# Kernel optimization log

Measured on AMD Instinct MI355X. Metric: run time of the kernel, lower is better.

The kernel has to match this reference:

```python
import jax, jax.numpy as jnp
import numpy as np

NEG_SLOPE = 0.2  # PyG GATConv default negative_slope


def gat_conv(h_in, src, dst, W, a_src, a_dst, bias, concat):
    """PyG GATConv: linear -> per-edge attention -> segment softmax -> scatter-add.
    h_in: [N, Fin]; W: [heads*C, Fin]; a_src/a_dst: [heads, C]; bias: [heads*C] or [C].
    add_self_loops=True (PyG default)."""
    N = h_in.shape[0]
    heads, C = a_src.shape
    loop = jnp.arange(N, dtype=src.dtype)
    s = jnp.concatenate([src, loop])
    d = jnp.concatenate([dst, loop])
    h = (h_in @ W.T).reshape(N, heads, C)          # [N, H, C]
    al_s = (h * a_src).sum(-1)                      # [N, H]
    al_d = (h * a_dst).sum(-1)                      # [N, H]
    e = jax.nn.leaky_relu(al_s[s] + al_d[d], NEG_SLOPE)  # [E, H]
    emax = jax.ops.segment_max(e, d, num_segments=N)     # every node has a self loop
    ex = jnp.exp(e - emax[d])
    denom = jax.ops.segment_sum(ex, d, num_segments=N)
    alpha = ex / denom[d]                           # [E, H]
    msg = alpha[:, :, None] * h[s]                  # [E, H, C]
    out = jax.ops.segment_sum(msg, d, num_segments=N)    # [N, H, C]
    if concat:
        out = out.reshape(N, heads * C)
    else:
        out = out.mean(axis=1)
    return out + bias


def setup_inputs() -> dict:
    key = jax.random.key(0)
    ks = jax.random.split(key, 14)
    B, N, T = 1, 20000, 4
    E = 320000
    HID, HEADS, OUT = 64, 4, 64
    sc = 0.1
    x = jax.random.normal(ks[0], (B, N, T), dtype=jnp.float32)
    edge_index = jax.random.randint(ks[1], (2, E), 0, N, dtype=jnp.int64)
    time_idx = jnp.arange(T, dtype=jnp.float32).reshape(T, 1)
    return {
        "x": x,
        "edge_index": edge_index,
        "time_idx": time_idx,
        "Wt": jax.random.normal(ks[2], (HID, 1), jnp.float32) * sc,
        "bt": jnp.zeros((HID,), jnp.float32),
        "Wf": jax.random.normal(ks[3], (HID, 1), jnp.float32) * sc,
        "bf": jnp.zeros((HID,), jnp.float32),
        "W1": jax.random.normal(ks[4], (HEADS * HID, HID), jnp.float32) * sc,
        "a_src1": jax.random.normal(ks[5], (HEADS, HID), jnp.float32) * sc,
        "a_dst1": jax.random.normal(ks[6], (HEADS, HID), jnp.float32) * sc,
        "b1": jnp.zeros((HEADS * HID,), jnp.float32),
        "temporal_attention": jnp.ones((T,), jnp.float32),
        "W2": jax.random.normal(ks[7], (OUT, HEADS * HID), jnp.float32) * sc,
        "a_src2": jax.random.normal(ks[8], (1, OUT), jnp.float32) * sc,
        "a_dst2": jax.random.normal(ks[9], (1, OUT), jnp.float32) * sc,
        "b2": jnp.zeros((OUT,), jnp.float32),
    }


def reference(x, edge_index, time_idx, Wt, bt, Wf, bf, W1, a_src1, a_dst1, b1,
              temporal_attention, W2, a_src2, a_dst2, b2):
    B, N, T = x.shape  # features dim == time_steps
    src, dst = edge_index[0], edge_index[1]
    time_emb = time_idx @ Wt.T + bt                 # [T, hidden]
    tw = jax.nn.softmax(temporal_attention)         # [T]
    combined = jnp.zeros((B * N, a_src1.shape[0] * a_src1.shape[1]), x.dtype)
    for t in range(T):  # small static time loop, as in original
        feats = x[:, :, t].reshape(-1, 1)           # [B*N, 1]
        emb = feats @ Wf.T + bf + time_emb[t]       # [B*N, hidden]
        h = gat_conv(emb, src, dst, W1, a_src1, a_dst1, b1, concat=True)
        combined = combined + tw[t] * jax.nn.relu(h)  # dropout is identity in eval
    out = gat_conv(combined, src, dst, W2, a_src2, a_dst2, b2, concat=False)
    return out.reshape(B, N, -1)
```

## Files before the change

kernel.cpp:

```cpp
#include <hip/hip_runtime.h>
#include <hip/hip_bf16.h>

#define NEG 0.2f
#define NELL 64

#define P_U   0
#define P_W   256
#define P_PS  1280
#define P_PD  1284
#define P_QS  1288
#define P_QD  1304
#define P_TW  1320
#define P_WT  1324
#define P_CNT 2560

typedef __bf16 bf16x8 __attribute__((ext_vector_type(8)));
typedef float  f32x4  __attribute__((ext_vector_type(4)));

__device__ __forceinline__ float lrelu(float v){ return v > 0.f ? v : NEG*v; }
__device__ __forceinline__ unsigned short f2bf(float f){
    unsigned u = __float_as_uint(f);
    unsigned r = u + 0x7fffu + ((u >> 16) & 1u);
    return (unsigned short)(r >> 16);
}

__global__ void preK(const float* time_idx, const float* Wt, const float* bt,
                     const float* Wf, const float* bf, const float* W1,
                     const float* as1, const float* ad1, const float* b1,
                     const float* ta, const float* W2,
                     float* P, unsigned short* W2bf, int* deg, int N)
{
    int tid = threadIdx.x;
    if (blockIdx.x != 0){
        int i0 = (blockIdx.x - 1)*256 + tid;
        int stride = (gridDim.x - 1)*256;
        for (int i = i0; i < N; i += stride) deg[i] = 0;
        for (int i = i0; i < 16384; i += stride) W2bf[i] = f2bf(W2[i]);
        return;
    }
    __shared__ float W1p[256][65];
    for (int i = tid; i < 16384; i += 256){
        int r = i >> 6, c = i & 63;
        W1p[r][c] = W1[i];
    }
    __syncthreads();
    const float* wrow = W1p[tid];
    float uu = 0.f;
    for (int k = 0; k < 64; ++k) uu += wrow[k]*Wf[k];
    P[P_U + tid] = uu;
    for (int t = 0; t < 4; ++t){
        float ti = time_idx[t];
        float vv = 0.f;
        for (int k = 0; k < 64; ++k) vv += wrow[k]*(bf[k] + ti*Wt[k] + bt[k]);
        P[P_W + t*256 + tid] = vv + b1[tid];
    }
    __syncthreads();
    if (tid < 4){
        int h = tid; float ps=0.f, pd=0.f;
        for (int c = 0; c < 64; ++c){
            float uv = P[P_U + h*64 + c];
            ps += uv * as1[h*64+c];
            pd += uv * ad1[h*64+c];
        }
        P[P_PS+h]=ps; P[P_PD+h]=pd;
    }
    if (tid < 16){
        int t = tid >> 2, h = tid & 3;
        float qs=0.f, qd=0.f;
        for (int c = 0; c < 64; ++c){
            float v = P[P_W + t*256 + h*64 + c] - b1[h*64+c];
            qs += v * as1[h*64+c];
            qd += v * ad1[h*64+c];
        }
        P[P_QS + t*4 + h] = qs;
        P[P_QD + t*4 + h] = qd;
    }
    if (tid == 0){
        float m = ta[0];
        for (int t = 1; t < 4; ++t) m = fmaxf(m, ta[t]);
        float s = 0.f, e[4];
        for (int t = 0; t < 4; ++t){ e[t] = __expf(ta[t]-m); s += e[t]; }
        for (int t = 0; t < 4; ++t) P[P_TW+t] = e[t]/s;
    }
    __syncthreads();
    for (int idx = tid; idx < 1024; idx += 256){
        int c = idx >> 2, t = idx & 3;
        P[P_WT + idx] = P[P_W + t*256 + c];
    }
}

__global__ void ellK(const int* ei, int E, int* deg, int* ell){
    int e = blockIdx.x*256 + threadIdx.x;
    if (e >= E) return;
    int d = ei[E+e];
    int pos = atomicAdd(&deg[d], 1);
    if (pos < NELL) ell[d*NELL + pos] = ei[e];
}

__launch_bounds__(256)
__global__ void gat1h2K(const float* x, const int* deg, const int* ell,
                        const float* P, const unsigned short* W2bfg,
                        const float* as2, const float* ad2,
                        unsigned short* h2bf, float* als2, float* ald2, int N)
{
    __shared__ unsigned short Abf[64*264];
    __shared__ float4 Sl[64][4];
    __shared__ float  Ul[256];
    __shared__ float4 WTl[256];
    __shared__ float  Pl[44];
    int tid = threadIdx.x;
    Ul[tid] = P[P_U + tid];
    WTl[tid] = reinterpret_cast<const float4*>(P + P_WT)[tid];
    if (tid < 44) Pl[tid] = P[P_PS + tid];
    __syncthreads();

    int nl = tid >> 2, t = tid & 3;
    int n  = blockIdx.x*64 + nl;
    {
        float s_out[4] = {0.f,0.f,0.f,0.f};
        if (n < N){
            float xn = x[n*4 + t];
            float ps[4], qsum[4], den[4], num[4];
            #pragma unroll
            for (int h = 0; h < 4; ++h){
                ps[h]   = Pl[h];
                qsum[h] = Pl[8 + t*4 + h] + xn*Pl[4 + h] + Pl[24 + t*4 + h];
                float ex = __expf(lrelu(xn*ps[h] + qsum[h]));
                den[h] = ex; num[h] = ex*xn;
            }
            int dgn = min(deg[n], NELL);
            const int* row = ell + n*NELL;
            int j = 0;
            for (; j + 4 <= dgn; j += 4){
                float v0 = x[row[j]*4 + t];
                float v1 = x[row[j+1]*4 + t];
                float v2 = x[row[j+2]*4 + t];
                float v3 = x[row[j+3]*4 + t];
                #pragma unroll
                for (int h = 0; h < 4; ++h){
                    float e0 = __expf(lrelu(v0*ps[h] + qsum[h]));
                    float e1 = __expf(lrelu(v1*ps[h] + qsum[h]));
                    float e2 = __expf(lrelu(v2*ps[h] + qsum[h]));
                    float e3 = __expf(lrelu(v3*ps[h] + qsum[h]));
                    den[h] += (e0 + e1) + (e2 + e3);
                    num[h] += e0*v0 + e1*v1 + e2*v2 + e3*v3;
                }
            }
            for (; j < dgn; ++j){
                float v = x[row[j]*4 + t];
                #pragma unroll
                for (int h = 0; h < 4; ++h){
                    float ex = __expf(lrelu(v*ps[h] + qsum[h]));
                    den[h] += ex; num[h] += ex*v;
                }
            }
            #pragma unroll
            for (int h = 0; h < 4; ++h) s_out[h] = num[h]/den[h];
        }
        #pragma unroll
        for (int h = 0; h < 4; ++h)
            reinterpret_cast<float*>(&Sl[nl][h])[t] = s_out[h];
    }
    __syncthreads();

    {
        float tw0 = Pl[40], tw1 = Pl[41], tw2 = Pl[42], tw3 = Pl[43];
        int q = t;
        float4 s4 = Sl[nl][q];
        unsigned int* arow = reinterpret_cast<unsigned int*>(&Abf[nl*264 + q*64]);
        #pragma unroll 8
        for (int jj = 0; jj < 64; jj += 2){
            int c = q*64 + jj;
            float4 wa = WTl[c], wb = WTl[c+1];
            float ua = Ul[c], ub = Ul[c+1];
            float v0 = tw0*fmaxf(s4.x*ua + wa.x, 0.f) + tw1*fmaxf(s4.y*ua + wa.y, 0.f)
                     + tw2*fmaxf(s4.z*ua + wa.z, 0.f) + tw3*fmaxf(s4.w*ua + wa.w, 0.f);
            float v1 = tw0*fmaxf(s4.x*ub + wb.x, 0.f) + tw1*fmaxf(s4.y*ub + wb.y, 0.f)
                     + tw2*fmaxf(s4.z*ub + wb.z, 0.f) + tw3*fmaxf(s4.w*ub + wb.w, 0.f);
            arow[jj>>1] = (unsigned)f2bf(v0) | ((unsigned)f2bf(v1) << 16);
        }
    }
    __syncthreads();

    int w = tid >> 6, lane = tid & 63, lr = lane & 15, lhi = lane >> 4;
    int r0 = w*16;
    bf16x8 a[8];
    #pragma unroll
    for (int kk = 0; kk < 8; ++kk)
        a[kk] = *reinterpret_cast<const bf16x8*>(&Abf[(r0+lr)*264 + kk*32 + lhi*8]);
    float s1[4] = {0.f,0.f,0.f,0.f}, s2[4] = {0.f,0.f,0.f,0.f};
    int gbase = blockIdx.x*64 + r0 + lhi*4;
    #pragma unroll
    for (int nt = 0; nt < 4; ++nt){
        f32x4 acc = {0.f,0.f,0.f,0.f};
        const unsigned short* bp = W2bfg + (nt*16 + lr)*256 + lhi*8;
        #pragma unroll
        for (int kk = 0; kk < 8; ++kk){
            bf16x8 b = *reinterpret_cast<const bf16x8*>(bp + kk*32);
            acc = __builtin_amdgcn_mfma_f32_16x16x32_bf16(a[kk], b, acc, 0, 0, 0);
        }
        float oas = as2[nt*16 + lr], oad = ad2[nt*16 + lr];
        #pragma unroll
        for (int r = 0; r < 4; ++r){
            int g = gbase + r;
            if (g < N) h2bf[(size_t)g*64 + nt*16 + lr] = f2bf(acc[r]);
            s1[r] += acc[r]*oas;
            s2[r] += acc[r]*oad;
        }
    }
    #pragma unroll
    for (int r = 0; r < 4; ++r){
        float v1 = s1[r], v2 = s2[r];
        #pragma unroll
        for (int off = 8; off > 0; off >>= 1){
            v1 += __shfl_xor(v1, off);
            v2 += __shfl_xor(v2, off);
        }
        int g = gbase + r;
        if (lr == 0 && g < N){ als2[g] = v1; ald2[g] = v2; }
    }
}

__launch_bounds__(256)
__global__ void attnpvK(const unsigned short* h2bf, const float* als2, const float* ald2,
                        const int* deg, const int* ell, const float* b2,
                        float* out, int N)
{
    __shared__ int   sbuf[8][32];
    __shared__ float wbuf[8][32];
    int hw = threadIdx.x >> 5, lane = threadIdx.x & 31;
    int n = blockIdx.x*8 + hw;
    if (n >= N) return;
    float aldn = ald2[n];
    int dgn = min(deg[n], NELL);
    const int* row = ell + n*NELL;
    float sw = __expf(lrelu(als2[n] + aldn));
    float den = sw;
    unsigned us = reinterpret_cast<const unsigned*>(h2bf + ((size_t)n<<6))[lane];
    float acc0 = sw * __uint_as_float(us << 16);
    float acc1 = sw * __uint_as_float(us & 0xffff0000u);
    for (int base = 0; base < dgn; base += 32){
        int cnt = min(32, dgn - base);
        int j = base + lane;
        int s = 0; float ex = 0.f;
        if (j < dgn){ s = row[j]; ex = __expf(lrelu(als2[s] + aldn)); }
        sbuf[hw][lane] = s; wbuf[hw][lane] = ex;
        float sx = ex;
        #pragma unroll
        for (int off = 16; off; off >>= 1) sx += __shfl_xor(sx, off);
        den += sx;
        int i = 0;
        for (; i + 4 <= cnt; i += 4){
            int   s0 = sbuf[hw][i],   s1 = sbuf[hw][i+1], s2 = sbuf[hw][i+2], s3 = sbuf[hw][i+3];
            float w0 = wbuf[hw][i],   w1 = wbuf[hw][i+1], w2 = wbuf[hw][i+2], w3 = wbuf[hw][i+3];
            unsigned g0 = reinterpret_cast<const unsigned*>(h2bf + ((size_t)s0<<6))[lane];
            unsigned g1 = reinterpret_cast<const unsigned*>(h2bf + ((size_t)s1<<6))[lane];
            unsigned g2 = reinterpret_cast<const unsigned*>(h2bf + ((size_t)s2<<6))[lane];
            unsigned g3 = reinterpret_cast<const unsigned*>(h2bf + ((size_t)s3<<6))[lane];
            acc0 += w0*__uint_as_float(g0 << 16);
            acc1 += w0*__uint_as_float(g0 & 0xffff0000u);
            acc0 += w1*__uint_as_float(g1 << 16);
            acc1 += w1*__uint_as_float(g1 & 0xffff0000u);
            acc0 += w2*__uint_as_float(g2 << 16);
            acc1 += w2*__uint_as_float(g2 & 0xffff0000u);
            acc0 += w3*__uint_as_float(g3 << 16);
            acc1 += w3*__uint_as_float(g3 & 0xffff0000u);
        }
        for (; i < cnt; ++i){
            float wv = wbuf[hw][i];
            unsigned g = reinterpret_cast<const unsigned*>(h2bf + ((size_t)sbuf[hw][i]<<6))[lane];
            acc0 += wv*__uint_as_float(g << 16);
            acc1 += wv*__uint_as_float(g & 0xffff0000u);
        }
    }
    float rd = 1.f/den;
    int c = lane*2;
    float2 o;
    o.x = acc0*rd + b2[c];
    o.y = acc1*rd + b2[c+1];
    reinterpret_cast<float2*>(out + (size_t)n*64)[lane] = o;
}

extern "C" void kernel_launch(void* const* d_in, const int* in_sizes, int n_in,
                              void* d_out, int out_size, void* d_ws, size_t ws_size,
                              hipStream_t stream)
{
    const float* x        = (const float*)d_in[0];
    const int*   ei       = (const int*)  d_in[1];
    const float* time_idx = (const float*)d_in[2];
    const float* Wt       = (const float*)d_in[3];
    const float* bt       = (const float*)d_in[4];
    const float* Wf       = (const float*)d_in[5];
    const float* bf       = (const float*)d_in[6];
    const float* W1       = (const float*)d_in[7];
    const float* as1      = (const float*)d_in[8];
    const float* ad1      = (const float*)d_in[9];
    const float* b1       = (const float*)d_in[10];
    const float* ta       = (const float*)d_in[11];
    const float* W2       = (const float*)d_in[12];
    const float* as2      = (const float*)d_in[13];
    const float* ad2      = (const float*)d_in[14];
    const float* b2       = (const float*)d_in[15];

    int N = in_sizes[0] / 4;
    int E = in_sizes[1] / 2;

    char* w = (char*)d_ws;
    auto al = [](size_t v){ return (v + 255) & ~(size_t)255; };
    size_t off = 0;
    float* P     = (float*)(w + off); off = al(off + P_CNT*sizeof(float));
    unsigned short* W2bf = (unsigned short*)(w + off); off = al(off + 16384*sizeof(unsigned short));
    int*   deg   = (int*)  (w + off); off = al(off + (size_t)N*sizeof(int));
    int*   ell   = (int*)  (w + off); off = al(off + (size_t)N*NELL*sizeof(int));
    unsigned short* h2bf = (unsigned short*)(w + off); off = al(off + (size_t)N*64*sizeof(unsigned short));
    float* als2  = (float*)(w + off); off = al(off + (size_t)N*sizeof(float));
    float* ald2  = (float*)(w + off); off = al(off + (size_t)N*sizeof(float));
    (void)off; (void)ws_size; (void)n_in; (void)out_size;

    preK<<<40, 256, 0, stream>>>(time_idx, Wt, bt, Wf, bf, W1, as1, ad1, b1, ta, W2, P, W2bf, deg, N);
    ellK<<<(E + 255)/256, 256, 0, stream>>>(ei, E, deg, ell);
    gat1h2K<<<(N + 63)/64, 256, 0, stream>>>(x, deg, ell, P, W2bf, as2, ad2, h2bf, als2, ald2, N);
    attnpvK<<<(N + 7)/8, 256, 0, stream>>>(h2bf, als2, ald2, deg, ell, b2, (float*)d_out, N);
}
```

Measured before the change: 73.40 us.

## Fuse ELL build, layer-1 GAT and layer-2 attention into one persistent kernel

Merges three kernels (ELL construction, the fused layer-1/h2 projection, and layer-2 attention aggregation) into a single kernel of 32-node tiles. Two hierarchical global barriers built from atomics, leaf counters plus a root, replace the kernel boundaries. Each block caches its tile's ELL rows and degrees in LDS and reuses its own als/ald values, which removes launch gaps and some global reloads. The grid barrier is only safe if all 625 blocks are co-resident, which launch_bounds(256,3) is meant to help with. If they are not, the spin guard can break out early and produce incorrect results, and the barriers themselves add spin overhead.

```diff
diff --git a/kernel.cpp b/kernel.cpp
--- a/kernel.cpp
+++ b/kernel.cpp
@@ -3,6 +3,10 @@
 
 #define NEG 0.2f
 #define NELL 64
+#define TILE 32
+#define NT 256
+#define NLEAF 64
+#define LSTRIDE 16
 
 #define P_U   0
 #define P_W   256
@@ -23,23 +27,45 @@
     unsigned r = u + 0x7fffu + ((u >> 16) & 1u);
     return (unsigned short)(r >> 16);
 }
+__device__ __forceinline__ float bflo(unsigned u){ return __uint_as_float(u << 16); }
+__device__ __forceinline__ float bfhi(unsigned u){ return __uint_as_float(u & 0xffff0000u); }
+
+__device__ __forceinline__ void gbar(int* leaf, int* root, int nblk, int phase){
+    __syncthreads();
+    if (threadIdx.x == 0){
+        __builtin_amdgcn_fence(__ATOMIC_RELEASE, "agent");
+        int li = blockIdx.x & (NLEAF-1);
+        int share = (nblk - li + NLEAF - 1) >> 6;
+        int lv = __hip_atomic_fetch_add(&leaf[li*LSTRIDE], 1, __ATOMIC_RELAXED, __HIP_MEMORY_SCOPE_AGENT) + 1;
+        if (lv == phase*share)
+            __hip_atomic_fetch_add(root, 1, __ATOMIC_RELAXED, __HIP_MEMORY_SCOPE_AGENT);
+        int guard = 0;
+        while (__hip_atomic_load(root, __ATOMIC_RELAXED, __HIP_MEMORY_SCOPE_AGENT) < phase*NLEAF){
+            __builtin_amdgcn_s_sleep(4);
+            if (++guard > 100000000) break;
+        }
+        __builtin_amdgcn_fence(__ATOMIC_ACQUIRE, "agent");
+    }
+    __syncthreads();
+}
 
 __global__ void preK(const float* time_idx, const float* Wt, const float* bt,
                      const float* Wf, const float* bf, const float* W1,
                      const float* as1, const float* ad1, const float* b1,
                      const float* ta, const float* W2,
-                     float* P, unsigned short* W2bf, int* deg, int N)
+                     float* P, unsigned short* W2bf, int* deg, int* barL, int N)
 {
     int tid = threadIdx.x;
     if (blockIdx.x != 0){
-        int i0 = (blockIdx.x - 1)*256 + tid;
-        int stride = (gridDim.x - 1)*256;
+        int i0 = (blockIdx.x - 1)*NT + tid;
+        int stride = (gridDim.x - 1)*NT;
         for (int i = i0; i < N; i += stride) deg[i] = 0;
+        for (int i = i0; i < NLEAF*LSTRIDE + 16; i += stride) barL[i] = 0;
         for (int i = i0; i < 16384; i += stride) W2bf[i] = f2bf(W2[i]);
         return;
     }
     __shared__ float W1p[256][65];
-    for (int i = tid; i < 16384; i += 256){
+    for (int i = tid; i < 16384; i += NT){
         int r = i >> 6, c = i & 63;
         W1p[r][c] = W1[i];
     }
@@ -83,202 +109,214 @@
         for (int t = 0; t < 4; ++t) P[P_TW+t] = e[t]/s;
     }
     __syncthreads();
-    for (int idx = tid; idx < 1024; idx += 256){
+    for (int idx = tid; idx < 1024; idx += NT){
         int c = idx >> 2, t = idx & 3;
         P[P_WT + idx] = P[P_W + t*256 + c];
     }
 }
 
-__global__ void ellK(const int* ei, int E, int* deg, int* ell){
-    int e = blockIdx.x*256 + threadIdx.x;
-    if (e >= E) return;
-    int d = ei[E+e];
-    int pos = atomicAdd(&deg[d], 1);
-    if (pos < NELL) ell[d*NELL + pos] = ei[e];
-}
-
-__launch_bounds__(256)
-__global__ void gat1h2K(const float* x, const int* deg, const int* ell,
-                        const float* P, const unsigned short* W2bfg,
-                        const float* as2, const float* ad2,
-                        unsigned short* h2bf, float* als2, float* ald2, int N)
+__global__ __launch_bounds__(NT, 3)
+void megaK(const float* x, const int* ei, int E, int N,
+           const float* P, const unsigned short* W2bfg,
+           const float* as2, const float* ad2, const float* b2,
+           int* deg, int* ell, unsigned short* h2bf, float* als2, float* ald2,
+           int* leaf, int* root, float* out, int nblk)
 {
-    __shared__ unsigned short Abf[64*264];
-    __shared__ float4 Sl[64][4];
+    __shared__ unsigned short Abf[TILE*264];
+    __shared__ float  Slf[TILE][4][4];
+    __shared__ float4 WTl[256];
     __shared__ float  Ul[256];
-    __shared__ float4 WTl[256];
     __shared__ float  Pl[44];
-    int tid = threadIdx.x;
+    __shared__ int    ellL[TILE][NELL];
+    __shared__ int    degL[TILE];
+    __shared__ float  redL[2][2][TILE];
+    __shared__ int    sbufB[8][32];
+    __shared__ float  wbufB[8][32];
+
+    int tid = threadIdx.x, bid = blockIdx.x;
+    int n0 = bid*TILE;
+
     Ul[tid] = P[P_U + tid];
     WTl[tid] = reinterpret_cast<const float4*>(P + P_WT)[tid];
     if (tid < 44) Pl[tid] = P[P_PS + tid];
-    __syncthreads();
-
-    int nl = tid >> 2, t = tid & 3;
-    int n  = blockIdx.x*64 + nl;
+
+    for (int e = bid*NT + tid; e < E; e += nblk*NT){
+        int d = ei[E+e];
+        int pos = atomicAdd(&deg[d], 1);
+        if (pos < NELL) ell[d*NELL + pos] = ei[e];
+    }
+    gbar(leaf, root, nblk, 1);
+
+    for (int i = tid; i < TILE*NELL; i += NT){
+        int r = i >> 6;
+        if (n0 + r < N) ellL[r][i & 63] = ell[(n0+r)*NELL + (i & 63)];
+    }
+    if (tid < TILE){
+        degL[tid] = (n0 + tid < N) ? min(deg[n0+tid], NELL) : 0;
+    }
+    __syncthreads();
+
     {
-        float s_out[4] = {0.f,0.f,0.f,0.f};
+        int nl = tid >> 3, t = (tid >> 1) & 3, hp = tid & 1;
+        int n = n0 + nl;
+        int h0 = hp*2, h1 = h0 + 1;
+        float o0 = 0.f, o1 = 0.f;
         if (n < N){
             float xn = x[n*4 + t];
-            float ps[4], qsum[4], den[4], num[4];
-            #pragma unroll
-            for (int h = 0; h < 4; ++h){
-                ps[h]   = Pl[h];
-                qsum[h] = Pl[8 + t*4 + h] + xn*Pl[4 + h] + Pl[24 + t*4 + h];
-                float ex = __expf(lrelu(xn*ps[h] + qsum[h]));
-                den[h] = ex; num[h] = ex*xn;
-            }
-            int dgn = min(deg[n], NELL);
-            const int* row = ell + n*NELL;
+            float ps0 = Pl[h0], ps1 = Pl[h1];
+            float q0 = Pl[8 + t*4 + h0] + xn*Pl[4 + h0] + Pl[24 + t*4 + h0];
+            float q1 = Pl[8 + t*4 + h1] + xn*Pl[4 + h1] + Pl[24 + t*4 + h1];
+            float e0 = __expf(lrelu(xn*ps0 + q0));
+            float e1 = __expf(lrelu(xn*ps1 + q1));
+            float den0 = e0, num0 = e0*xn, den1 = e1, num1 = e1*xn;
+            int dgn = degL[nl];
             int j = 0;
             for (; j + 4 <= dgn; j += 4){
-                float v0 = x[row[j]*4 + t];
-                float v1 = x[row[j+1]*4 + t];
-                float v2 = x[row[j+2]*4 + t];
-                float v3 = x[row[j+3]*4 + t];
-                #pragma unroll
-                for (int h = 0; h < 4; ++h){
-                    float e0 = __expf(lrelu(v0*ps[h] + qsum[h]));
-                    float e1 = __expf(lrelu(v1*ps[h] + qsum[h]));
-                    float e2 = __expf(lrelu(v2*ps[h] + qsum[h]));
-                    float e3 = __expf(lrelu(v3*ps[h] + qsum[h]));
-                    den[h] += (e0 + e1) + (e2 + e3);
-                    num[h] += e0*v0 + e1*v1 + e2*v2 + e3*v3;
-                }
+                int s0 = ellL[nl][j], s1 = ellL[nl][j+1], s2 = ellL[nl][j+2], s3 = ellL[nl][j+3];
+                float v0 = x[s0*4 + t], v1 = x[s1*4 + t], v2 = x[s2*4 + t], v3 = x[s3*4 + t];
+                float a0 = __expf(lrelu(v0*ps0 + q0)), c0 = __expf(lrelu(v0*ps1 + q1));
+                float a1 = __expf(lrelu(v1*ps0 + q0)), c1 = __expf(lrelu(v1*ps1 + q1));
+                float a2 = __expf(lrelu(v2*ps0 + q0)), c2 = __expf(lrelu(v2*ps1 + q1));
+                float a3 = __expf(lrelu(v3*ps0 + q0)), c3 = __expf(lrelu(v3*ps1 + q1));
+                den0 += (a0 + a1) + (a2 + a3);
+                num0 += a0*v0 + a1*v1 + a2*v2 + a3*v3;
+                den1 += (c0 + c1) + (c2 + c3);
+                num1 += c0*v0 + c1*v1 + c2*v2 + c3*v3;
             }
             for (; j < dgn; ++j){
-                float v = x[row[j]*4 + t];
-                #pragma unroll
-                for (int h = 0; h < 4; ++h){
-                    float ex = __expf(lrelu(v*ps[h] + qsum[h]));
-                    den[h] += ex; num[h] += ex*v;
-                }
-            }
-            #pragma unroll
-            for (int h = 0; h < 4; ++h) s_out[h] = num[h]/den[h];
-        }
-        #pragma unroll
-        for (int h = 0; h < 4; ++h)
-            reinterpret_cast<float*>(&Sl[nl][h])[t] = s_out[h];
+                float v = x[ellL[nl][j]*4 + t];
+                float a = __expf(lrelu(v*ps0 + q0)), c = __expf(lrelu(v*ps1 + q1));
+                den0 += a; num0 += a*v;
+                den1 += c; num1 += c*v;
+            }
+            o0 = num0/den0; o1 = num1/den1;
+        }
+        Slf[nl][h0][t] = o0;
+        Slf[nl][h1][t] = o1;
     }
     __syncthreads();
 
     {
+        int nl = tid >> 3, q = tid & 7;
         float tw0 = Pl[40], tw1 = Pl[41], tw2 = Pl[42], tw3 = Pl[43];
-        int q = t;
-        float4 s4 = Sl[nl][q];
-        unsigned int* arow = reinterpret_cast<unsigned int*>(&Abf[nl*264 + q*64]);
+        unsigned* arow = reinterpret_cast<unsigned*>(&Abf[nl*264 + q*32]);
         #pragma unroll 8
-        for (int jj = 0; jj < 64; jj += 2){
-            int c = q*64 + jj;
+        for (int jj = 0; jj < 32; jj += 2){
+            int c = q*32 + jj;
+            int h = c >> 6;
+            float sx = Slf[nl][h][0], sy = Slf[nl][h][1], sz = Slf[nl][h][2], sw = Slf[nl][h][3];
             float4 wa = WTl[c], wb = WTl[c+1];
             float ua = Ul[c], ub = Ul[c+1];
-            float v0 = tw0*fmaxf(s4.x*ua + wa.x, 0.f) + tw1*fmaxf(s4.y*ua + wa.y, 0.f)
-                     + tw2*fmaxf(s4.z*ua + wa.z, 0.f) + tw3*fmaxf(s4.w*ua + wa.w, 0.f);
-            float v1 = tw0*fmaxf(s4.x*ub + wb.x, 0.f) + tw1*fmaxf(s4.y*ub + wb.y, 0.f)
-                     + tw2*fmaxf(s4.z*ub + wb.z, 0.f) + tw3*fmaxf(s4.w*ub + wb.w, 0.f);
+            float v0 = tw0*fmaxf(sx*ua + wa.x, 0.f) + tw1*fmaxf(sy*ua + wa.y, 0.f)
+                     + tw2*fmaxf(sz*ua + wa.z, 0.f) + tw3*fmaxf(sw*ua + wa.w, 0.f);
+            float v1 = tw0*fmaxf(sx*ub + wb.x, 0.f) + tw1*fmaxf(sy*ub + wb.y, 0.f)
+                     + tw2*fmaxf(sz*ub + wb.z, 0.f) + tw3*fmaxf(sw*ub + wb.w, 0.f);
             arow[jj>>1] = (unsigned)f2bf(v0) | ((unsigned)f2bf(v1) << 16);
         }
     }
     __syncthreads();
 
-    int w = tid >> 6, lane = tid & 63, lr = lane & 15, lhi = lane >> 4;
-    int r0 = w*16;
-    bf16x8 a[8];
-    #pragma unroll
-    for (int kk = 0; kk < 8; ++kk)
-        a[kk] = *reinterpret_cast<const bf16x8*>(&Abf[(r0+lr)*264 + kk*32 + lhi*8]);
-    float s1[4] = {0.f,0.f,0.f,0.f}, s2[4] = {0.f,0.f,0.f,0.f};
-    int gbase = blockIdx.x*64 + r0 + lhi*4;
-    #pragma unroll
-    for (int nt = 0; nt < 4; ++nt){
-        f32x4 acc = {0.f,0.f,0.f,0.f};
-        const unsigned short* bp = W2bfg + (nt*16 + lr)*256 + lhi*8;
+    {
+        int w = tid >> 6, lane = tid & 63, lr = lane & 15, lhi = lane >> 4;
+        int rg = w & 1, cg = w >> 1;
+        bf16x8 a[8];
         #pragma unroll
-        for (int kk = 0; kk < 8; ++kk){
-            bf16x8 b = *reinterpret_cast<const bf16x8*>(bp + kk*32);
-            acc = __builtin_amdgcn_mfma_f32_16x16x32_bf16(a[kk], b, acc, 0, 0, 0);
-        }
-        float oas = as2[nt*16 + lr], oad = ad2[nt*16 + lr];
+        for (int kk = 0; kk < 8; ++kk)
+            a[kk] = *reinterpret_cast<const bf16x8*>(&Abf[(rg*16 + lr)*264 + kk*32 + lhi*8]);
+        float s1[4] = {0.f,0.f,0.f,0.f}, s2[4] = {0.f,0.f,0.f,0.f};
+        #pragma unroll
+        for (int nt2 = 0; nt2 < 2; ++nt2){
+            int nt = cg*2 + nt2;
+            f32x4 acc = {0.f,0.f,0.f,0.f};
+            const unsigned short* bp = W2bfg + (nt*16 + lr)*256 + lhi*8;
+            #pragma unroll
+            for (int kk = 0; kk < 8; ++kk){
+                bf16x8 b = *reinterpret_cast<const bf16x8*>(bp + kk*32);
+                acc = __builtin_amdgcn_mfma_f32_16x16x32_bf16(a[kk], b, acc, 0, 0, 0);
+            }
+            int o = nt*16 + lr;
+            float oas = as2[o], oad = ad2[o];
+            #pragma unroll
+            for (int r = 0; r < 4; ++r){
+                int g = n0 + rg*16 + lhi*4 + r;
+                if (g < N) h2bf[(size_t)g*64 + o] = f2bf(acc[r]);
+                s1[r] += acc[r]*oas;
+                s2[r] += acc[r]*oad;
+            }
+        }
         #pragma unroll
         for (int r = 0; r < 4; ++r){
-            int g = gbase + r;
-            if (g < N) h2bf[(size_t)g*64 + nt*16 + lr] = f2bf(acc[r]);
-            s1[r] += acc[r]*oas;
-            s2[r] += acc[r]*oad;
-        }
-    }
-    #pragma unroll
-    for (int r = 0; r < 4; ++r){
-        float v1 = s1[r], v2 = s2[r];
-        #pragma unroll
-        for (int off = 8; off > 0; off >>= 1){
-            v1 += __shfl_xor(v1, off);
-            v2 += __shfl_xor(v2, off);
-        }
-        int g = gbase + r;
-        if (lr == 0 && g < N){ als2[g] = v1; ald2[g] = v2; }
-    }
-}
-
-__launch_bounds__(256)
-__global__ void attnpvK(const unsigned short* h2bf, const float* als2, const float* ald2,
-                        const int* deg, const int* ell, const float* b2,
-                        float* out, int N)
-{
-    __shared__ int   sbuf[8][32];
-    __shared__ float wbuf[8][32];
-    int hw = threadIdx.x >> 5, lane = threadIdx.x & 31;
-    int n = blockIdx.x*8 + hw;
-    if (n >= N) return;
-    float aldn = ald2[n];
-    int dgn = min(deg[n], NELL);
-    const int* row = ell + n*NELL;
-    float sw = __expf(lrelu(als2[n] + aldn));
-    float den = sw;
-    unsigned us = reinterpret_cast<const unsigned*>(h2bf + ((size_t)n<<6))[lane];
-    float acc0 = sw * __uint_as_float(us << 16);
-    float acc1 = sw * __uint_as_float(us & 0xffff0000u);
-    for (int base = 0; base < dgn; base += 32){
-        int cnt = min(32, dgn - base);
-        int j = base + lane;
-        int s = 0; float ex = 0.f;
-        if (j < dgn){ s = row[j]; ex = __expf(lrelu(als2[s] + aldn)); }
-        sbuf[hw][lane] = s; wbuf[hw][lane] = ex;
-        float sx = ex;
-        #pragma unroll
-        for (int off = 16; off; off >>= 1) sx += __shfl_xor(sx, off);
-        den += sx;
-        int i = 0;
-        for (; i + 4 <= cnt; i += 4){
-            int   s0 = sbuf[hw][i],   s1 = sbuf[hw][i+1], s2 = sbuf[hw][i+2], s3 = sbuf[hw][i+3];
-            float w0 = wbuf[hw][i],   w1 = wbuf[hw][i+1], w2 = wbuf[hw][i+2], w3 = wbuf[hw][i+3];
-            unsigned g0 = reinterpret_cast<const unsigned*>(h2bf + ((size_t)s0<<6))[lane];
-            unsigned g1 = reinterpret_cast<const unsigned*>(h2bf + ((size_t)s1<<6))[lane];
-            unsigned g2 = reinterpret_cast<const unsigned*>(h2bf + ((size_t)s2<<6))[lane];
-            unsigned g3 = reinterpret_cast<const unsigned*>(h2bf + ((size_t)s3<<6))[lane];
-            acc0 += w0*__uint_as_float(g0 << 16);
-            acc1 += w0*__uint_as_float(g0 & 0xffff0000u);
-            acc0 += w1*__uint_as_float(g1 << 16);
-            acc1 += w1*__uint_as_float(g1 & 0xffff0000u);
-            acc0 += w2*__uint_as_float(g2 << 16);
-            acc1 += w2*__uint_as_float(g2 & 0xffff0000u);
-            acc0 += w3*__uint_as_float(g3 << 16);
-            acc1 += w3*__uint_as_float(g3 & 0xffff0000u);
-        }
-        for (; i < cnt; ++i){
-            float wv = wbuf[hw][i];
-            unsigned g = reinterpret_cast<const unsigned*>(h2bf + ((size_t)sbuf[hw][i]<<6))[lane];
-            acc0 += wv*__uint_as_float(g << 16);
-            acc1 += wv*__uint_as_float(g & 0xffff0000u);
-        }
-    }
-    float rd = 1.f/den;
-    int c = lane*2;
-    float2 o;
-    o.x = acc0*rd + b2[c];
-    o.y = acc1*rd + b2[c+1];
-    reinterpret_cast<float2*>(out + (size_t)n*64)[lane] = o;
+            float v1 = s1[r], v2 = s2[r];
+            #pragma unroll
+            for (int off = 8; off > 0; off >>= 1){
+                v1 += __shfl_xor(v1, off);
+                v2 += __shfl_xor(v2, off);
+            }
+            if (lr == 0){
+                redL[0][cg][rg*16 + lhi*4 + r] = v1;
+                redL[1][cg][rg*16 + lhi*4 + r] = v2;
+            }
+        }
+    }
+    __syncthreads();
+    if (tid < TILE && n0 + tid < N){
+        als2[n0 + tid] = redL[0][0][tid] + redL[0][1][tid];
+        ald2[n0 + tid] = redL[1][0][tid] + redL[1][1][tid];
+    }
+
+    gbar(leaf, root, nblk, 2);
+
+    {
+        int hw = tid >> 5, lane = tid & 31;
+        for (int k = 0; k < 4; ++k){
+            int nl = hw*4 + k;
+            int n = n0 + nl;
+            if (n >= N) continue;
+            float asn  = redL[0][0][nl] + redL[0][1][nl];
+            float aldn = redL[1][0][nl] + redL[1][1][nl];
+            int dgn = degL[nl];
+            float sw = __expf(lrelu(asn + aldn));
+            float den = sw;
+            unsigned us = *reinterpret_cast<const unsigned*>(h2bf + ((size_t)n << 6) + lane*2);
+            float acc0 = sw * bflo(us);
+            float acc1 = sw * bfhi(us);
+            for (int base = 0; base < dgn; base += 32){
+                int cnt = min(32, dgn - base);
+                int j = base + lane;
+                int s = 0; float ex = 0.f;
+                if (j < dgn){ s = ellL[nl][j]; ex = __expf(lrelu(als2[s] + aldn)); }
+                sbufB[hw][lane] = s; wbufB[hw][lane] = ex;
+                float sx = ex;
+                #pragma unroll
+                for (int off = 16; off; off >>= 1) sx += __shfl_xor(sx, off);
+                den += sx;
+                int i = 0;
+                for (; i + 4 <= cnt; i += 4){
+                    int   s0 = sbufB[hw][i],   s1 = sbufB[hw][i+1], s2 = sbufB[hw][i+2], s3 = sbufB[hw][i+3];
+                    float w0 = wbufB[hw][i],   w1 = wbufB[hw][i+1], w2 = wbufB[hw][i+2], w3 = wbufB[hw][i+3];
+                    unsigned g0 = *reinterpret_cast<const unsigned*>(h2bf + ((size_t)s0 << 6) + lane*2);
+                    unsigned g1 = *reinterpret_cast<const unsigned*>(h2bf + ((size_t)s1 << 6) + lane*2);
+                    unsigned g2 = *reinterpret_cast<const unsigned*>(h2bf + ((size_t)s2 << 6) + lane*2);
+                    unsigned g3 = *reinterpret_cast<const unsigned*>(h2bf + ((size_t)s3 << 6) + lane*2);
+                    acc0 += w0*bflo(g0); acc1 += w0*bfhi(g0);
+                    acc0 += w1*bflo(g1); acc1 += w1*bfhi(g1);
+                    acc0 += w2*bflo(g2); acc1 += w2*bfhi(g2);
+                    acc0 += w3*bflo(g3); acc1 += w3*bfhi(g3);
+                }
+                for (; i < cnt; ++i){
+                    float wv = wbufB[hw][i];
+                    unsigned g = *reinterpret_cast<const unsigned*>(h2bf + ((size_t)sbufB[hw][i] << 6) + lane*2);
+                    acc0 += wv*bflo(g); acc1 += wv*bfhi(g);
+                }
+            }
+            float rd = 1.f/den;
+            int c = lane*2;
+            float2 o;
+            o.x = acc0*rd + b2[c];
+            o.y = acc1*rd + b2[c+1];
+            reinterpret_cast<float2*>(out + (size_t)n*64)[lane] = o;
+        }
+    }
 }
 
 extern "C" void kernel_launch(void* const* d_in, const int* in_sizes, int n_in,
@@ -315,10 +353,15 @@
     unsigned short* h2bf = (unsigned short*)(w + off); off = al(off + (size_t)N*64*sizeof(unsigned short));
     float* als2  = (float*)(w + off); off = al(off + (size_t)N*sizeof(float));
     float* ald2  = (float*)(w + off); off = al(off + (size_t)N*sizeof(float));
+    int*   barL  = (int*)  (w + off); off = al(off + (NLEAF*LSTRIDE + 16)*sizeof(int));
+    int*   rootp = barL + NLEAF*LSTRIDE;
     (void)off; (void)ws_size; (void)n_in; (void)out_size;
 
-    preK<<<40, 256, 0, stream>>>(time_idx, Wt, bt, Wf, bf, W1, as1, ad1, b1, ta, W2, P, W2bf, deg, N);
-    ellK<<<(E + 255)/256, 256, 0, stream>>>(ei, E, deg, ell);
-    gat1h2K<<<(N + 63)/64, 256, 0, stream>>>(x, deg, ell, P, W2bf, as2, ad2, h2bf, als2, ald2, N);
-    attnpvK<<<(N + 7)/8, 256, 0, stream>>>(h2bf, als2, ald2, deg, ell, b2, (float*)d_out, N);
-}
+    int ntiles = (N + TILE - 1)/TILE;
+
+    preK<<<40, NT, 0, stream>>>(time_idx, Wt, bt, Wf, bf, W1, as1, ad1, b1, ta, W2,
+                                P, W2bf, deg, barL, N);
+    megaK<<<ntiles, NT, 0, stream>>>(x, ei, E, N, P, W2bf, as2, ad2, b2,
+                                     deg, ell, h2bf, als2, ald2,
+                                     barL, rootp, (float*)d_out, ntiles);
+}
```

Measured after the change: 126.7 us. 1.73x slower.

## Double threads per block in fused GAT layer-1/h2 kernel, splitting edges and columns

Applied to the files above, without the earlier changes.

The fused layer-1 aggregation plus h2 GEMM kernel now runs 512 threads per 64-node block instead of 256. In the aggregation, two threads share each (node, time) pair and take alternating edges, then combine partial sums with a shuffle. The combine stage writes 32 columns per thread instead of 64, and the MFMA stage splits output column tiles across two wave groups, with a shared-memory reduction for the attention scalars. The aim is more parallelism and latency hiding for the gather-heavy phase, at the cost of an extra barrier and shuffles.

```diff
diff --git a/kernel.cpp b/kernel.cpp
--- a/kernel.cpp
+++ b/kernel.cpp
@@ -23,6 +23,8 @@
     unsigned r = u + 0x7fffu + ((u >> 16) & 1u);
     return (unsigned short)(r >> 16);
 }
+__device__ __forceinline__ float bflo(unsigned u){ return __uint_as_float(u << 16); }
+__device__ __forceinline__ float bfhi(unsigned u){ return __uint_as_float(u & 0xffff0000u); }
 
 __global__ void preK(const float* time_idx, const float* Wt, const float* bt,
                      const float* Wf, const float* bf, const float* W1,
@@ -97,27 +99,31 @@
     if (pos < NELL) ell[d*NELL + pos] = ei[e];
 }
 
-__launch_bounds__(256)
+__launch_bounds__(512)
 __global__ void gat1h2K(const float* x, const int* deg, const int* ell,
                         const float* P, const unsigned short* W2bfg,
                         const float* as2, const float* ad2,
                         unsigned short* h2bf, float* als2, float* ald2, int N)
 {
     __shared__ unsigned short Abf[64*264];
-    __shared__ float4 Sl[64][4];
+    __shared__ float  Slf[64][4][4];
     __shared__ float  Ul[256];
     __shared__ float4 WTl[256];
     __shared__ float  Pl[44];
+    __shared__ float  redL[2][2][64];
     int tid = threadIdx.x;
-    Ul[tid] = P[P_U + tid];
-    WTl[tid] = reinterpret_cast<const float4*>(P + P_WT)[tid];
-    if (tid < 44) Pl[tid] = P[P_PS + tid];
-    __syncthreads();
-
-    int nl = tid >> 2, t = tid & 3;
+    if (tid < 256){
+        Ul[tid] = P[P_U + tid];
+        WTl[tid] = reinterpret_cast<const float4*>(P + P_WT)[tid];
+        if (tid < 44) Pl[tid] = P[P_PS + tid];
+    }
+    __syncthreads();
+
+    int nl = tid >> 3, sub = tid & 7, t = sub >> 1, half = sub & 1;
     int n  = blockIdx.x*64 + nl;
+
     {
-        float s_out[4] = {0.f,0.f,0.f,0.f};
+        float o[4] = {0.f,0.f,0.f,0.f};
         if (n < N){
             float xn = x[n*4 + t];
             float ps[4], qsum[4], den[4], num[4];
@@ -125,17 +131,17 @@
             for (int h = 0; h < 4; ++h){
                 ps[h]   = Pl[h];
                 qsum[h] = Pl[8 + t*4 + h] + xn*Pl[4 + h] + Pl[24 + t*4 + h];
-                float ex = __expf(lrelu(xn*ps[h] + qsum[h]));
-                den[h] = ex; num[h] = ex*xn;
+                if (half == 0){
+                    float ex = __expf(lrelu(xn*ps[h] + qsum[h]));
+                    den[h] = ex; num[h] = ex*xn;
+                } else { den[h] = 0.f; num[h] = 0.f; }
             }
             int dgn = min(deg[n], NELL);
             const int* row = ell + n*NELL;
-            int j = 0;
-            for (; j + 4 <= dgn; j += 4){
-                float v0 = x[row[j]*4 + t];
-                float v1 = x[row[j+1]*4 + t];
-                float v2 = x[row[j+2]*4 + t];
-                float v3 = x[row[j+3]*4 + t];
+            int j = half;
+            for (; j + 6 < dgn; j += 8){
+                int s0 = row[j], s1 = row[j+2], s2 = row[j+4], s3 = row[j+6];
+                float v0 = x[s0*4 + t], v1 = x[s1*4 + t], v2 = x[s2*4 + t], v3 = x[s3*4 + t];
                 #pragma unroll
                 for (int h = 0; h < 4; ++h){
                     float e0 = __expf(lrelu(v0*ps[h] + qsum[h]));
@@ -146,7 +152,7 @@
                     num[h] += e0*v0 + e1*v1 + e2*v2 + e3*v3;
                 }
             }
-            for (; j < dgn; ++j){
+            for (; j < dgn; j += 2){
                 float v = x[row[j]*4 + t];
                 #pragma unroll
                 for (int h = 0; h < 4; ++h){
@@ -155,69 +161,86 @@
                 }
             }
             #pragma unroll
-            for (int h = 0; h < 4; ++h) s_out[h] = num[h]/den[h];
-        }
-        #pragma unroll
-        for (int h = 0; h < 4; ++h)
-            reinterpret_cast<float*>(&Sl[nl][h])[t] = s_out[h];
+            for (int h = 0; h < 4; ++h){
+                float d = den[h] + __shfl_xor(den[h], 1);
+                float m = num[h] + __shfl_xor(num[h], 1);
+                o[h] = m/d;
+            }
+        }
+        if (half == 0){
+            #pragma unroll
+            for (int h = 0; h < 4; ++h) Slf[nl][h][t] = o[h];
+        }
     }
     __syncthreads();
 
     {
+        int q = sub;
+        int h = q >> 1;
         float tw0 = Pl[40], tw1 = Pl[41], tw2 = Pl[42], tw3 = Pl[43];
-        int q = t;
-        float4 s4 = Sl[nl][q];
-        unsigned int* arow = reinterpret_cast<unsigned int*>(&Abf[nl*264 + q*64]);
+        float sx = Slf[nl][h][0], sy = Slf[nl][h][1], sz = Slf[nl][h][2], sw = Slf[nl][h][3];
+        unsigned* arow = reinterpret_cast<unsigned*>(&Abf[nl*264 + q*32]);
         #pragma unroll 8
-        for (int jj = 0; jj < 64; jj += 2){
-            int c = q*64 + jj;
+        for (int jj = 0; jj < 32; jj += 2){
+            int c = q*32 + jj;
             float4 wa = WTl[c], wb = WTl[c+1];
             float ua = Ul[c], ub = Ul[c+1];
-            float v0 = tw0*fmaxf(s4.x*ua + wa.x, 0.f) + tw1*fmaxf(s4.y*ua + wa.y, 0.f)
-                     + tw2*fmaxf(s4.z*ua + wa.z, 0.f) + tw3*fmaxf(s4.w*ua + wa.w, 0.f);
-            float v1 = tw0*fmaxf(s4.x*ub + wb.x, 0.f) + tw1*fmaxf(s4.y*ub + wb.y, 0.f)
-                     + tw2*fmaxf(s4.z*ub + wb.z, 0.f) + tw3*fmaxf(s4.w*ub + wb.w, 0.f);
+            float v0 = tw0*fmaxf(sx*ua + wa.x, 0.f) + tw1*fmaxf(sy*ua + wa.y, 0.f)
+                     + tw2*fmaxf(sz*ua + wa.z, 0.f) + tw3*fmaxf(sw*ua + wa.w, 0.f);
+            float v1 = tw0*fmaxf(sx*ub + wb.x, 0.f) + tw1*fmaxf(sy*ub + wb.y, 0.f)
+                     + tw2*fmaxf(sz*ub + wb.z, 0.f) + tw3*fmaxf(sw*ub + wb.w, 0.f);
             arow[jj>>1] = (unsigned)f2bf(v0) | ((unsigned)f2bf(v1) << 16);
         }
     }
     __syncthreads();
 
-    int w = tid >> 6, lane = tid & 63, lr = lane & 15, lhi = lane >> 4;
-    int r0 = w*16;
-    bf16x8 a[8];
-    #pragma unroll
-    for (int kk = 0; kk < 8; ++kk)
-        a[kk] = *reinterpret_cast<const bf16x8*>(&Abf[(r0+lr)*264 + kk*32 + lhi*8]);
-    float s1[4] = {0.f,0.f,0.f,0.f}, s2[4] = {0.f,0.f,0.f,0.f};
-    int gbase = blockIdx.x*64 + r0 + lhi*4;
-    #pragma unroll
-    for (int nt = 0; nt < 4; ++nt){
-        f32x4 acc = {0.f,0.f,0.f,0.f};
-        const unsigned short* bp = W2bfg + (nt*16 + lr)*256 + lhi*8;
+    {
+        int w = tid >> 6, lane = tid & 63, lr = lane & 15, lhi = lane >> 4;
+        int rg = w & 3, cg = w >> 2;
+        bf16x8 a[8];
         #pragma unroll
-        for (int kk = 0; kk < 8; ++kk){
-            bf16x8 b = *reinterpret_cast<const bf16x8*>(bp + kk*32);
-            acc = __builtin_amdgcn_mfma_f32_16x16x32_bf16(a[kk], b, acc, 0, 0, 0);
-        }
-        float oas = as2[nt*16 + lr], oad = ad2[nt*16 + lr];
+        for (int kk = 0; kk < 8; ++kk)
+            a[kk] = *reinterpret_cast<const bf16x8*>(&Abf[(rg*16 + lr)*264 + kk*32 + lhi*8]);
+        float s1[4] = {0.f,0.f,0.f,0.f}, s2[4] = {0.f,0.f,0.f,0.f};
+        int gbase = blockIdx.x*64 + rg*16 + lhi*4;
+        #pragma unroll
+        for (int nt2 = 0; nt2 < 2; ++nt2){
+            int nt = cg*2 + nt2;
+            f32x4 acc = {0.f,0.f,0.f,0.f};
+            const unsigned short* bp = W2bfg + (nt*16 + lr)*256 + lhi*8;
+            #pragma unroll
+            for (int kk = 0; kk < 8; ++kk){
+                bf16x8 b = *reinterpret_cast<const bf16x8*>(bp + kk*32);
+                acc = __builtin_amdgcn_mfma_f32_16x16x32_bf16(a[kk], b, acc, 0, 0, 0);
+            }
+            int o = nt*16 + lr;
+            float oas = as2[o], oad = ad2[o];
+            #pragma unroll
+            for (int r = 0; r < 4; ++r){
+                int g = gbase + r;
+                if (g < N) h2bf[(size_t)g*64 + o] = f2bf(acc[r]);
+                s1[r] += acc[r]*oas;
+                s2[r] += acc[r]*oad;
+            }
+        }
         #pragma unroll
         for (int r = 0; r < 4; ++r){
-            int g = gbase + r;
-            if (g < N) h2bf[(size_t)g*64 + nt*16 + lr] = f2bf(acc[r]);
-            s1[r] += acc[r]*oas;
-            s2[r] += acc[r]*oad;
-        }
-    }
-    #pragma unroll
-    for (int r = 0; r < 4; ++r){
-        float v1 = s1[r], v2 = s2[r];
-        #pragma unroll
-        for (int off = 8; off > 0; off >>= 1){
-            v1 += __shfl_xor(v1, off);
-            v2 += __shfl_xor(v2, off);
-        }
-        int g = gbase + r;
-        if (lr == 0 && g < N){ als2[g] = v1; ald2[g] = v2; }
+            float v1 = s1[r], v2 = s2[r];
+            #pragma unroll
+            for (int off = 8; off > 0; off >>= 1){
+                v1 += __shfl_xor(v1, off);
+                v2 += __shfl_xor(v2, off);
+            }
+            if (lr == 0){
+                redL[0][cg][rg*16 + lhi*4 + r] = v1;
+                redL[1][cg][rg*16 + lhi*4 + r] = v2;
+            }
+        }
+    }
+    __syncthreads();
+    if (tid < 64 && blockIdx.x*64 + tid < N){
+        als2[blockIdx.x*64 + tid] = redL[0][0][tid] + redL[0][1][tid];
+        ald2[blockIdx.x*64 + tid] = redL[1][0][tid] + redL[1][1][tid];
     }
 }
 
@@ -237,8 +260,8 @@
     float sw = __expf(lrelu(als2[n] + aldn));
     float den = sw;
     unsigned us = reinterpret_cast<const unsigned*>(h2bf + ((size_t)n<<6))[lane];
-    float acc0 = sw * __uint_as_float(us << 16);
-    float acc1 = sw * __uint_as_float(us & 0xffff0000u);
+    float acc0 = sw * bflo(us);
+    float acc1 = sw * bfhi(us);
     for (int base = 0; base < dgn; base += 32){
         int cnt = min(32, dgn - base);
         int j = base + lane;
@@ -257,20 +280,15 @@
             unsigned g1 = reinterpret_cast<const unsigned*>(h2bf + ((size_t)s1<<6))[lane];
             unsigned g2 = reinterpret_cast<const unsigned*>(h2bf + ((size_t)s2<<6))[lane];
             unsigned g3 = reinterpret_cast<const unsigned*>(h2bf + ((size_t)s3<<6))[lane];
-            acc0 += w0*__uint_as_float(g0 << 16);
-            acc1 += w0*__uint_as_float(g0 & 0xffff0000u);
-            acc0 += w1*__uint_as_float(g1 << 16);
-            acc1 += w1*__uint_as_float(g1 & 0xffff0000u);
-            acc0 += w2*__uint_as_float(g2 << 16);
-            acc1 += w2*__uint_as_float(g2 & 0xffff0000u);
-            acc0 += w3*__uint_as_float(g3 << 16);
-            acc1 += w3*__uint_as_float(g3 & 0xffff0000u);
+            acc0 += w0*bflo(g0); acc1 += w0*bfhi(g0);
+            acc0 += w1*bflo(g1); acc1 += w1*bfhi(g1);
+            acc0 += w2*bflo(g2); acc1 += w2*bfhi(g2);
+            acc0 += w3*bflo(g3); acc1 += w3*bfhi(g3);
         }
         for (; i < cnt; ++i){
             float wv = wbuf[hw][i];
             unsigned g = reinterpret_cast<const unsigned*>(h2bf + ((size_t)sbuf[hw][i]<<6))[lane];
-            acc0 += wv*__uint_as_float(g << 16);
-            acc1 += wv*__uint_as_float(g & 0xffff0000u);
+            acc0 += wv*bflo(g); acc1 += wv*bfhi(g);
         }
     }
     float rd = 1.f/den;
@@ -319,6 +337,6 @@
 
     preK<<<40, 256, 0, stream>>>(time_idx, Wt, bt, Wf, bf, W1, as1, ad1, b1, ta, W2, P, W2bf, deg, N);
     ellK<<<(E + 255)/256, 256, 0, stream>>>(ei, E, deg, ell);
-    gat1h2K<<<(N + 63)/64, 256, 0, stream>>>(x, deg, ell, P, W2bf, as2, ad2, h2bf, als2, ald2, N);
+    gat1h2K<<<(N + 63)/64, 512, 0, stream>>>(x, deg, ell, P, W2bf, as2, ad2, h2bf, als2, ald2, N);
     attnpvK<<<(N + 7)/8, 256, 0, stream>>>(h2bf, als2, ald2, deg, ell, b2, (float*)d_out, N);
 }
```

After: 75.57 us. +3.0%, slower.

## Merge ELL build with parameter precompute into one kernel, split out deg zeroing

Applied to the files above, without the earlier changes.

The degree-zeroing step moves into a small dedicated kernel. The ELL adjacency build, the W1 parameter precompute and the W2 bf16 conversion now run as different block ranges of one launch, so the serial single-block precompute overlaps the edge scatter instead of running before it. The precompute is also reworked to read W1 rows directly with float4 loads against small LDS vectors rather than staging a padded copy of W1 in shared memory. Launch count stays the same, but the kernel-boundary dependency between the precompute and the ELL build is removed.

```diff
diff --git a/kernel.cpp b/kernel.cpp
--- a/kernel.cpp
+++ b/kernel.cpp
@@ -23,50 +23,76 @@
     unsigned r = u + 0x7fffu + ((u >> 16) & 1u);
     return (unsigned short)(r >> 16);
 }
-
-__global__ void preK(const float* time_idx, const float* Wt, const float* bt,
-                     const float* Wf, const float* bf, const float* W1,
-                     const float* as1, const float* ad1, const float* b1,
-                     const float* ta, const float* W2,
-                     float* P, unsigned short* W2bf, int* deg, int N)
+__device__ __forceinline__ float bflo(unsigned u){ return __uint_as_float(u << 16); }
+__device__ __forceinline__ float bfhi(unsigned u){ return __uint_as_float(u & 0xffff0000u); }
+
+__global__ void zeroK(int* deg, int N){
+    int i = blockIdx.x*256 + threadIdx.x;
+    if (i < N) deg[i] = 0;
+}
+
+__global__ void ellpreK(const int* ei, int E, int* deg, int* ell,
+                        const float* time_idx, const float* Wt, const float* bt,
+                        const float* Wf, const float* bf, const float* W1,
+                        const float* as1, const float* ad1, const float* b1,
+                        const float* ta, const float* W2,
+                        float* P, unsigned short* W2bf, int EB)
 {
-    int tid = threadIdx.x;
-    if (blockIdx.x != 0){
-        int i0 = (blockIdx.x - 1)*256 + tid;
-        int stride = (gridDim.x - 1)*256;
-        for (int i = i0; i < N; i += stride) deg[i] = 0;
-        for (int i = i0; i < 16384; i += stride) W2bf[i] = f2bf(W2[i]);
+    int tid = threadIdx.x, bid = blockIdx.x;
+    if (bid < EB){
+        int e = bid*256 + tid;
+        if (e < E){
+            int d = ei[E+e];
+            int pos = atomicAdd(&deg[d], 1);
+            if (pos < NELL) ell[d*NELL + pos] = ei[e];
+        }
         return;
     }
-    __shared__ float W1p[256][65];
-    for (int i = tid; i < 16384; i += 256){
-        int r = i >> 6, c = i & 63;
-        W1p[r][c] = W1[i];
-    }
-    __syncthreads();
-    const float* wrow = W1p[tid];
-    float uu = 0.f;
-    for (int k = 0; k < 64; ++k) uu += wrow[k]*Wf[k];
-    P[P_U + tid] = uu;
-    for (int t = 0; t < 4; ++t){
-        float ti = time_idx[t];
-        float vv = 0.f;
-        for (int k = 0; k < 64; ++k) vv += wrow[k]*(bf[k] + ti*Wt[k] + bt[k]);
-        P[P_W + t*256 + tid] = vv + b1[tid];
+    if (bid > EB){
+        int i0 = (bid - EB - 1)*256 + tid;
+        for (int i = i0; i < 16384; i += 40*256) W2bf[i] = f2bf(W2[i]);
+        return;
+    }
+    __shared__ float Zl[5][64];
+    if (tid < 64){
+        float wtk = Wt[tid], btk = bt[tid], bfk = bf[tid];
+        Zl[0][tid] = Wf[tid];
+        #pragma unroll
+        for (int t = 0; t < 4; ++t)
+            Zl[1+t][tid] = bfk + time_idx[t]*wtk + btk;
+    }
+    __syncthreads();
+    {
+        const float* wrow = W1 + tid*64;
+        float uu = 0.f, v0 = 0.f, v1 = 0.f, v2 = 0.f, v3 = 0.f;
+        for (int k = 0; k < 64; k += 4){
+            float4 w4 = *reinterpret_cast<const float4*>(wrow + k);
+            uu += w4.x*Zl[0][k] + w4.y*Zl[0][k+1] + w4.z*Zl[0][k+2] + w4.w*Zl[0][k+3];
+            v0 += w4.x*Zl[1][k] + w4.y*Zl[1][k+1] + w4.z*Zl[1][k+2] + w4.w*Zl[1][k+3];
+            v1 += w4.x*Zl[2][k] + w4.y*Zl[2][k+1] + w4.z*Zl[2][k+2] + w4.w*Zl[2][k+3];
+            v2 += w4.x*Zl[3][k] + w4.y*Zl[3][k+1] + w4.z*Zl[3][k+2] + w4.w*Zl[3][k+3];
+            v3 += w4.x*Zl[4][k] + w4.y*Zl[4][k+1] + w4.z*Zl[4][k+2] + w4.w*Zl[4][k+3];
+        }
+        float b = b1[tid];
+        P[P_U + tid] = uu;
+        P[P_W + 0*256 + tid] = v0 + b;
+        P[P_W + 1*256 + tid] = v1 + b;
+        P[P_W + 2*256 + tid] = v2 + b;
+        P[P_W + 3*256 + tid] = v3 + b;
     }
     __syncthreads();
     if (tid < 4){
-        int h = tid; float ps=0.f, pd=0.f;
+        int h = tid; float ps = 0.f, pd = 0.f;
         for (int c = 0; c < 64; ++c){
             float uv = P[P_U + h*64 + c];
             ps += uv * as1[h*64+c];
             pd += uv * ad1[h*64+c];
         }
-        P[P_PS+h]=ps; P[P_PD+h]=pd;
+        P[P_PS+h] = ps; P[P_PD+h] = pd;
     }
     if (tid < 16){
         int t = tid >> 2, h = tid & 3;
-        float qs=0.f, qd=0.f;
+        float qs = 0.f, qd = 0.f;
         for (int c = 0; c < 64; ++c){
             float v = P[P_W + t*256 + h*64 + c] - b1[h*64+c];
             qs += v * as1[h*64+c];
@@ -87,14 +113,6 @@
         int c = idx >> 2, t = idx & 3;
         P[P_WT + idx] = P[P_W + t*256 + c];
     }
-}
-
-__global__ void ellK(const int* ei, int E, int* deg, int* ell){
-    int e = blockIdx.x*256 + threadIdx.x;
-    if (e >= E) return;
-    int d = ei[E+e];
-    int pos = atomicAdd(&deg[d], 1);
-    if (pos < NELL) ell[d*NELL + pos] = ei[e];
 }
 
 __launch_bounds__(256)
@@ -237,8 +255,8 @@
     float sw = __expf(lrelu(als2[n] + aldn));
     float den = sw;
     unsigned us = reinterpret_cast<const unsigned*>(h2bf + ((size_t)n<<6))[lane];
-    float acc0 = sw * __uint_as_float(us << 16);
-    float acc1 = sw * __uint_as_float(us & 0xffff0000u);
+    float acc0 = sw * bflo(us);
+    float acc1 = sw * bfhi(us);
     for (int base = 0; base < dgn; base += 32){
         int cnt = min(32, dgn - base);
         int j = base + lane;
@@ -257,20 +275,15 @@
             unsigned g1 = reinterpret_cast<const unsigned*>(h2bf + ((size_t)s1<<6))[lane];
             unsigned g2 = reinterpret_cast<const unsigned*>(h2bf + ((size_t)s2<<6))[lane];
             unsigned g3 = reinterpret_cast<const unsigned*>(h2bf + ((size_t)s3<<6))[lane];
-            acc0 += w0*__uint_as_float(g0 << 16);
-            acc1 += w0*__uint_as_float(g0 & 0xffff0000u);
-            acc0 += w1*__uint_as_float(g1 << 16);
-            acc1 += w1*__uint_as_float(g1 & 0xffff0000u);
-            acc0 += w2*__uint_as_float(g2 << 16);
-            acc1 += w2*__uint_as_float(g2 & 0xffff0000u);
-            acc0 += w3*__uint_as_float(g3 << 16);
-            acc1 += w3*__uint_as_float(g3 & 0xffff0000u);
+            acc0 += w0*bflo(g0); acc1 += w0*bfhi(g0);
+            acc0 += w1*bflo(g1); acc1 += w1*bfhi(g1);
+            acc0 += w2*bflo(g2); acc1 += w2*bfhi(g2);
+            acc0 += w3*bflo(g3); acc1 += w3*bfhi(g3);
         }
         for (; i < cnt; ++i){
             float wv = wbuf[hw][i];
             unsigned g = reinterpret_cast<const unsigned*>(h2bf + ((size_t)sbuf[hw][i]<<6))[lane];
-            acc0 += wv*__uint_as_float(g << 16);
-            acc1 += wv*__uint_as_float(g & 0xffff0000u);
+            acc0 += wv*bflo(g); acc1 += wv*bfhi(g);
         }
     }
     float rd = 1.f/den;
@@ -317,8 +330,12 @@
     float* ald2  = (float*)(w + off); off = al(off + (size_t)N*sizeof(float));
     (void)off; (void)ws_size; (void)n_in; (void)out_size;
 
-    preK<<<40, 256, 0, stream>>>(time_idx, Wt, bt, Wf, bf, W1, as1, ad1, b1, ta, W2, P, W2bf, deg, N);
-    ellK<<<(E + 255)/256, 256, 0, stream>>>(ei, E, deg, ell);
+    int EB = (E + 255)/256;
+
+    zeroK<<<(N + 255)/256, 256, 0, stream>>>(deg, N);
+    ellpreK<<<EB + 41, 256, 0, stream>>>(ei, E, deg, ell,
+                                         time_idx, Wt, bt, Wf, bf, W1, as1, ad1, b1, ta, W2,
+                                         P, W2bf, EB);
     gat1h2K<<<(N + 63)/64, 256, 0, stream>>>(x, deg, ell, P, W2bf, as2, ad2, h2bf, als2, ald2, N);
     attnpvK<<<(N + 7)/8, 256, 0, stream>>>(h2bf, als2, ald2, deg, ell, b2, (float*)d_out, N);
 }
```

Result: faster. 65.53 us (-10.7%).
